# Kernel optimization log

Hardware: AMD Instinct MI355X
Metric: run time of the kernel (lower is better)

The kernel has to match this reference:

```python
import jax, jax.numpy as jnp
import numpy as np

BITS = 12
MB = BITS - 1                      # mantissa bits
MAX_VAL = 1.0 - 2.0 ** (-MB)       # superfloat max representable magnitude
DENOM = float(2 ** MB - 1)


def sf_decode(enc):
    # enc: int32. NOTE: faithful to source, including its sign convention
    # decoded * (2*sign - 1) where sign=1 for negative inputs (flips sign).
    mantissa = enc & ((1 << MB) - 1)
    sign = (enc >> MB) & 1
    mag = mantissa.astype(jnp.float32) / DENOM * MAX_VAL
    return mag * (2 * sign - 1).astype(jnp.float32)


def sf_encode(x):
    c = jnp.clip(x, -MAX_VAL, MAX_VAL)
    oor = jnp.abs(x) > MAX_VAL
    mantissa = jnp.floor(jnp.abs(c) * DENOM / MAX_VAL).astype(jnp.int32)
    sign = (c < 0).astype(jnp.int32)
    return (mantissa | (sign << MB)), oor


def setup_inputs() -> dict:
    key = jax.random.key(0)
    k1, k2, k3, k4, k5 = jax.random.split(key, 5)
    T, IN, OUT = 512, 4096, 11008
    x = jax.random.normal(k1, (T, IN), dtype=jnp.float32)
    weight_full = jax.random.normal(k2, (OUT, IN), dtype=jnp.float32) * 0.02
    scale = jnp.ones((OUT,), dtype=jnp.float32)
    bias = jax.random.normal(k3, (OUT,), dtype=jnp.float32) * 0.01
    encoded_weight = jax.random.randint(k4, (OUT, IN), 0, 2 ** BITS, dtype=jnp.int32)
    outlier_mask = jax.random.uniform(k5, (OUT, IN)) < 0.005
    return {"x": x, "weight_full": weight_full, "scale": scale, "bias": bias,
            "encoded_weight": encoded_weight, "outlier_mask": outlier_mask}


def reference(x, weight_full, scale, bias, encoded_weight, outlier_mask):
    # decode packed superfloat weight, scatter outliers, rescale per-row
    w = sf_decode(encoded_weight)                       # [OUT, IN]
    w = jnp.where(outlier_mask, weight_full, w)         # == w[mask] = weight[mask]
    w = w * scale[:, None]
    # quantize activations (encode then decode)
    enc_x, _ = sf_encode(x)
    xq = sf_decode(enc_x)                               # [T, IN]
    return xq @ w.T + bias                              # [T, OUT]
```

## Files before the change

### kernel.cpp

```cpp
#include <hip/hip_runtime.h>
#include <hip/hip_bf16.h>
#include <stdint.h>

#define T_DIM 512
#define IN_DIM 4096
#define OUT_DIM 11008

typedef __attribute__((ext_vector_type(8))) __bf16 bf16x8;
typedef __attribute__((ext_vector_type(8))) short shortx8;
typedef __attribute__((ext_vector_type(4))) float f32x4;
typedef __attribute__((ext_vector_type(4))) int intx4;

__device__ __forceinline__ short f32_to_bf16_bits(float f) {
    uint32_t x = __builtin_bit_cast(uint32_t, f);
    x += 0x7FFFu + ((x >> 16) & 1u);
    return (short)(x >> 16);
}

__global__ __launch_bounds__(256) void encode_x_kernel(const float* __restrict__ x,
                                                       short* __restrict__ xq) {
    const float MAXV = 2047.0f / 2048.0f;
    int i = (blockIdx.x * 256 + threadIdx.x) * 8;
    float4 a = *(const float4*)(x + i);
    float4 b = *(const float4*)(x + i + 4);
    float v[8] = {a.x, a.y, a.z, a.w, b.x, b.y, b.z, b.w};
    union { short s[8]; intx4 v4; } u;
#pragma unroll
    for (int j = 0; j < 8; ++j) {
        float xv = v[j];
        float ax = fminf(fabsf(xv), MAXV);
        float m = floorf(ax * 2047.0f / MAXV);
        float q = m * (1.0f / 2048.0f) * (xv < 0.0f ? 1.0f : -1.0f);
        u.s[j] = f32_to_bf16_bits(q);
    }
    *(intx4*)(xq + i) = u.v4;
}

__global__ __launch_bounds__(256) void decode_w_kernel(const int* __restrict__ enc,
                                                       const int* __restrict__ mask,
                                                       const float* __restrict__ wf,
                                                       short* __restrict__ wq) {
    size_t i = (size_t)(blockIdx.x * 256 + threadIdx.x) * 16;
    intx4 e[4], m[4];
#pragma unroll
    for (int j = 0; j < 4; ++j) e[j] = *(const intx4*)(enc + i + 4 * j);
#pragma unroll
    for (int j = 0; j < 4; ++j) m[j] = *(const intx4*)(mask + i + 4 * j);
    const int* ev = (const int*)e;
    const int* mk = (const int*)m;
    union { short s[16]; intx4 v4[2]; } u;
#pragma unroll
    for (int j = 0; j < 16; ++j) {
        int v12 = ev[j];
        float v = (float)(v12 & 2047) * (1.0f / 2048.0f) * (((v12 >> 11) & 1) ? 1.0f : -1.0f);
        if (mk[j]) v = wf[i + j];
        u.s[j] = f32_to_bf16_bits(v);
    }
    __builtin_nontemporal_store(u.v4[0], (intx4*)(wq + i));
    __builtin_nontemporal_store(u.v4[1], (intx4*)(wq + i + 8));
}

#define BM 128
#define BN 128
#define BK 32
#define KITERS (IN_DIM / BK)

__global__ __launch_bounds__(256) void gemm_bt_kernel(const short* __restrict__ A,
                                                      const short* __restrict__ B,
                                                      const float* __restrict__ scale,
                                                      const float* __restrict__ bias,
                                                      float* __restrict__ C) {
    __shared__ short As[BM * BK];
    __shared__ short Bs[BN * BK];
    const int tid  = threadIdx.x;
    const int wave = tid >> 6;
    const int lane = tid & 63;
    const int bn = blockIdx.x, bm = blockIdx.y;

    const int f0 = tid * 8;
    const int r0 = f0 >> 5, c0 = f0 & 31;
    const int f1 = (256 + tid) * 8;
    const int r1 = f1 >> 5, c1 = f1 & 31;
    const short* gA0 = A + (size_t)(bm * BM + r0) * IN_DIM + c0;
    const short* gA1 = A + (size_t)(bm * BM + r1) * IN_DIM + c1;
    const short* gB0 = B + (size_t)(bn * BN + r0) * IN_DIM + c0;
    const short* gB1 = B + (size_t)(bn * BN + r1) * IN_DIM + c1;
    short* lA0 = As + (wave * 64) * 8;
    short* lA1 = As + (256 + wave * 64) * 8;
    short* lB0 = Bs + (wave * 64) * 8;
    short* lB1 = Bs + (256 + wave * 64) * 8;

    const int wm = (wave >> 1) * 64;
    const int wn = (wave & 1) * 64;
    const int quad = lane >> 4;
    const int lr   = lane & 15;

    f32x4 acc[4][4] = {};

    for (int kt = 0; kt < KITERS; ++kt) {
        const int ko = kt * BK;
        __builtin_amdgcn_global_load_lds((__attribute__((address_space(1))) void*)(gA0 + ko),
                                         (__attribute__((address_space(3))) void*)lA0, 16, 0, 0);
        __builtin_amdgcn_global_load_lds((__attribute__((address_space(1))) void*)(gA1 + ko),
                                         (__attribute__((address_space(3))) void*)lA1, 16, 0, 0);
        __builtin_amdgcn_global_load_lds((__attribute__((address_space(1))) void*)(gB0 + ko),
                                         (__attribute__((address_space(3))) void*)lB0, 16, 0, 0);
        __builtin_amdgcn_global_load_lds((__attribute__((address_space(1))) void*)(gB1 + ko),
                                         (__attribute__((address_space(3))) void*)lB1, 16, 0, 0);
        __syncthreads();

        bf16x8 af[4], bfr[4];
#pragma unroll
        for (int mi = 0; mi < 4; ++mi)
            af[mi] = __builtin_bit_cast(bf16x8,
                *(const shortx8*)(As + (wm + mi * 16 + lr) * BK + quad * 8));
#pragma unroll
        for (int ni = 0; ni < 4; ++ni)
            bfr[ni] = __builtin_bit_cast(bf16x8,
                *(const shortx8*)(Bs + (wn + ni * 16 + lr) * BK + quad * 8));
#pragma unroll
        for (int mi = 0; mi < 4; ++mi)
#pragma unroll
            for (int ni = 0; ni < 4; ++ni)
                acc[mi][ni] = __builtin_amdgcn_mfma_f32_16x16x32_bf16(
                    af[mi], bfr[ni], acc[mi][ni], 0, 0, 0);
        __syncthreads();
    }

    const int rowb = bm * BM + wm + quad * 4;
    const int colb = bn * BN + wn + lr;
#pragma unroll
    for (int ni = 0; ni < 4; ++ni) {
        const int col = colb + ni * 16;
        const float sv = scale[col];
        const float bv = bias[col];
#pragma unroll
        for (int mi = 0; mi < 4; ++mi) {
#pragma unroll
            for (int r = 0; r < 4; ++r) {
                const int row = rowb + mi * 16 + r;
                C[(size_t)row * OUT_DIM + col] = acc[mi][ni][r] * sv + bv;
            }
        }
    }
}

extern "C" void kernel_launch(void* const* d_in, const int* in_sizes, int n_in,
                              void* d_out, int out_size, void* d_ws, size_t ws_size,
                              hipStream_t stream) {
    const float* x     = (const float*)d_in[0];
    const float* wf    = (const float*)d_in[1];
    const float* scale = (const float*)d_in[2];
    const float* bias  = (const float*)d_in[3];
    const int*   enc   = (const int*)d_in[4];
    const int*   mask  = (const int*)d_in[5];
    float* out = (float*)d_out;

    short* xq = (short*)d_ws;
    short* wq = (short*)d_ws + (size_t)T_DIM * IN_DIM;

    encode_x_kernel<<<(T_DIM * IN_DIM) / (256 * 8), 256, 0, stream>>>(x, xq);
    decode_w_kernel<<<((size_t)OUT_DIM * IN_DIM) / (256 * 16), 256, 0, stream>>>(
        enc, mask, wf, wq);
    dim3 grid(OUT_DIM / BN, T_DIM / BM);
    gemm_bt_kernel<<<grid, 256, 0, stream>>>(xq, wq, scale, bias, out);
}
```

Baseline: 562.7 us.

## Fuse weight decoding into GEMM B-tile loading, drop separate decode pass

```diff
diff --git a/kernel.cpp b/kernel.cpp
--- a/kernel.cpp
+++ b/kernel.cpp
@@ -36,46 +36,26 @@
     *(intx4*)(xq + i) = u.v4;
 }
 
-__global__ __launch_bounds__(256) void decode_w_kernel(const int* __restrict__ enc,
-                                                       const int* __restrict__ mask,
-                                                       const float* __restrict__ wf,
-                                                       short* __restrict__ wq) {
-    size_t i = (size_t)(blockIdx.x * 256 + threadIdx.x) * 16;
-    intx4 e[4], m[4];
-#pragma unroll
-    for (int j = 0; j < 4; ++j) e[j] = *(const intx4*)(enc + i + 4 * j);
-#pragma unroll
-    for (int j = 0; j < 4; ++j) m[j] = *(const intx4*)(mask + i + 4 * j);
-    const int* ev = (const int*)e;
-    const int* mk = (const int*)m;
-    union { short s[16]; intx4 v4[2]; } u;
-#pragma unroll
-    for (int j = 0; j < 16; ++j) {
-        int v12 = ev[j];
-        float v = (float)(v12 & 2047) * (1.0f / 2048.0f) * (((v12 >> 11) & 1) ? 1.0f : -1.0f);
-        if (mk[j]) v = wf[i + j];
-        u.s[j] = f32_to_bf16_bits(v);
-    }
-    __builtin_nontemporal_store(u.v4[0], (intx4*)(wq + i));
-    __builtin_nontemporal_store(u.v4[1], (intx4*)(wq + i + 8));
-}
-
 #define BM 128
-#define BN 128
+#define BN 64
 #define BK 32
+#define BNP 40
 #define KITERS (IN_DIM / BK)
 
-__global__ __launch_bounds__(256) void gemm_bt_kernel(const short* __restrict__ A,
-                                                      const short* __restrict__ B,
-                                                      const float* __restrict__ scale,
-                                                      const float* __restrict__ bias,
-                                                      float* __restrict__ C) {
+__global__ __launch_bounds__(256) void fused_gemm_kernel(const short* __restrict__ A,
+                                                         const int* __restrict__ enc,
+                                                         const int* __restrict__ mask,
+                                                         const float* __restrict__ wf,
+                                                         const float* __restrict__ scale,
+                                                         const float* __restrict__ bias,
+                                                         float* __restrict__ C) {
     __shared__ short As[BM * BK];
-    __shared__ short Bs[BN * BK];
+    __shared__ short Bs[BN * BNP];
     const int tid  = threadIdx.x;
     const int wave = tid >> 6;
     const int lane = tid & 63;
-    const int bn = blockIdx.x, bm = blockIdx.y;
+    const int bm = blockIdx.x;
+    const int bn = blockIdx.y;
 
     const int f0 = tid * 8;
     const int r0 = f0 >> 5, c0 = f0 & 31;
@@ -83,19 +63,28 @@
     const int r1 = f1 >> 5, c1 = f1 & 31;
     const short* gA0 = A + (size_t)(bm * BM + r0) * IN_DIM + c0;
     const short* gA1 = A + (size_t)(bm * BM + r1) * IN_DIM + c1;
-    const short* gB0 = B + (size_t)(bn * BN + r0) * IN_DIM + c0;
-    const short* gB1 = B + (size_t)(bn * BN + r1) * IN_DIM + c1;
     short* lA0 = As + (wave * 64) * 8;
     short* lA1 = As + (256 + wave * 64) * 8;
-    short* lB0 = Bs + (wave * 64) * 8;
-    short* lB1 = Bs + (256 + wave * 64) * 8;
+
+    const int rB = tid >> 2;
+    const int cB = (tid & 3) * 8;
+    const size_t goff = (size_t)(bn * BN + rB) * IN_DIM + cB;
+    const int* encp = enc + goff;
+    const int* mskp = mask + goff;
+    const float* wfp = wf + goff;
+    short* sB = Bs + rB * BNP + cB;
 
     const int wm = (wave >> 1) * 64;
-    const int wn = (wave & 1) * 64;
+    const int wn = (wave & 1) * 32;
     const int quad = lane >> 4;
     const int lr   = lane & 15;
 
-    f32x4 acc[4][4] = {};
+    f32x4 acc[4][2] = {};
+
+    intx4 e0 = *(const intx4*)(encp);
+    intx4 e1 = *(const intx4*)(encp + 4);
+    intx4 m0 = *(const intx4*)(mskp);
+    intx4 m1 = *(const intx4*)(mskp + 4);
 
     for (int kt = 0; kt < KITERS; ++kt) {
         const int ko = kt * BK;
@@ -103,25 +92,40 @@
                                          (__attribute__((address_space(3))) void*)lA0, 16, 0, 0);
         __builtin_amdgcn_global_load_lds((__attribute__((address_space(1))) void*)(gA1 + ko),
                                          (__attribute__((address_space(3))) void*)lA1, 16, 0, 0);
-        __builtin_amdgcn_global_load_lds((__attribute__((address_space(1))) void*)(gB0 + ko),
-                                         (__attribute__((address_space(3))) void*)lB0, 16, 0, 0);
-        __builtin_amdgcn_global_load_lds((__attribute__((address_space(1))) void*)(gB1 + ko),
-                                         (__attribute__((address_space(3))) void*)lB1, 16, 0, 0);
+        int ev[8] = {e0.x, e0.y, e0.z, e0.w, e1.x, e1.y, e1.z, e1.w};
+        int mk[8] = {m0.x, m0.y, m0.z, m0.w, m1.x, m1.y, m1.z, m1.w};
+        union { short s[8]; intx4 v4; } u;
+#pragma unroll
+        for (int j = 0; j < 8; ++j) {
+            int v12 = ev[j];
+            float v = (float)(v12 & 2047) * (1.0f / 2048.0f) * (((v12 >> 11) & 1) ? 1.0f : -1.0f);
+            if (mk[j]) v = wfp[ko + j];
+            u.s[j] = f32_to_bf16_bits(v);
+        }
+        *(intx4*)sB = u.v4;
         __syncthreads();
 
-        bf16x8 af[4], bfr[4];
+        if (kt + 1 < KITERS) {
+            const int kn = ko + BK;
+            e0 = *(const intx4*)(encp + kn);
+            e1 = *(const intx4*)(encp + kn + 4);
+            m0 = *(const intx4*)(mskp + kn);
+            m1 = *(const intx4*)(mskp + kn + 4);
+        }
+
+        bf16x8 af[4], bfr[2];
 #pragma unroll
         for (int mi = 0; mi < 4; ++mi)
             af[mi] = __builtin_bit_cast(bf16x8,
                 *(const shortx8*)(As + (wm + mi * 16 + lr) * BK + quad * 8));
 #pragma unroll
-        for (int ni = 0; ni < 4; ++ni)
+        for (int ni = 0; ni < 2; ++ni)
             bfr[ni] = __builtin_bit_cast(bf16x8,
-                *(const shortx8*)(Bs + (wn + ni * 16 + lr) * BK + quad * 8));
+                *(const shortx8*)(Bs + (wn + ni * 16 + lr) * BNP + quad * 8));
 #pragma unroll
         for (int mi = 0; mi < 4; ++mi)
 #pragma unroll
-            for (int ni = 0; ni < 4; ++ni)
+            for (int ni = 0; ni < 2; ++ni)
                 acc[mi][ni] = __builtin_amdgcn_mfma_f32_16x16x32_bf16(
                     af[mi], bfr[ni], acc[mi][ni], 0, 0, 0);
         __syncthreads();
@@ -130,7 +134,7 @@
     const int rowb = bm * BM + wm + quad * 4;
     const int colb = bn * BN + wn + lr;
 #pragma unroll
-    for (int ni = 0; ni < 4; ++ni) {
+    for (int ni = 0; ni < 2; ++ni) {
         const int col = colb + ni * 16;
         const float sv = scale[col];
         const float bv = bias[col];
@@ -157,11 +161,8 @@
     float* out = (float*)d_out;
 
     short* xq = (short*)d_ws;
-    short* wq = (short*)d_ws + (size_t)T_DIM * IN_DIM;
 
     encode_x_kernel<<<(T_DIM * IN_DIM) / (256 * 8), 256, 0, stream>>>(x, xq);
-    decode_w_kernel<<<((size_t)OUT_DIM * IN_DIM) / (256 * 16), 256, 0, stream>>>(
-        enc, mask, wf, wq);
-    dim3 grid(OUT_DIM / BN, T_DIM / BM);
-    gemm_bt_kernel<<<grid, 256, 0, stream>>>(xq, wq, scale, bias, out);
+    dim3 grid(T_DIM / BM, OUT_DIM / BN);
+    fused_gemm_kernel<<<grid, 256, 0, stream>>>(xq, enc, mask, wf, scale, bias, out);
 }
```

Measured after the change: 628.7 us. 11.7% more time.
